# Kernel tuning notes

Measured on AMD Instinct MI355X. Metric: run time of the kernel, lower is better.

Reference implementation:

```python
import jax, jax.numpy as jnp
import numpy as np

B, P, D = 64, 196, 2048      # batch, num_pixels, encoder_dim
E, H, A = 512, 512, 512      # embed, hidden, attention dims
V, S = 32000, 22             # vocab, caption seq_len


def setup_inputs() -> dict:
    key = jax.random.key(0)
    ks = jax.random.split(key, 24)
    sc = 0.02
    features = jax.random.normal(ks[0], (B, P, D), jnp.float32)
    captions = jax.random.randint(ks[1], (S, B), 0, V)
    caption_lengths = jax.random.randint(ks[2], (B,), 3, S + 1)
    caption_lengths = caption_lengths.at[0].set(S)  # make max static = S
    p = lambda i, shp: sc * jax.random.normal(ks[i], shp, jnp.float32)
    return {
        "features": features,
        "captions": captions,
        "caption_lengths": caption_lengths,
        "emb_W": p(3, (V, E)),
        "We": p(4, (D, A)), "be": p(5, (A,)),
        "Wd": p(6, (H, A)), "bd": p(7, (A,)),
        "wf": p(8, (A, 1)), "bf": p(9, (1,)),
        "Wih": p(10, (4 * H, E + D)), "Whh": p(11, (4 * H, H)),
        "bih": p(12, (4 * H,)), "bhh": p(13, (4 * H,)),
        "Wh0": p(14, (D, H)), "bh0": p(15, (H,)),
        "Wc0": p(16, (D, H)), "bc0": p(17, (H,)),
        "Wbeta": p(18, (H, D)), "bbeta": p(19, (D,)),
        "Wout": p(20, (H, V)), "bout": p(21, (V,)),
    }


def reference(features, captions, caption_lengths, emb_W, We, be, Wd, bd, wf, bf,
              Wih, Whh, bih, bhh, Wh0, bh0, Wc0, bc0, Wbeta, bbeta, Wout, bout):
    # sort batch by caption length, descending
    sort_ind = jnp.argsort(-caption_lengths)
    lens = caption_lengths[sort_ind]
    enc = features[sort_ind]                     # [B,P,D]
    caps = captions.T[sort_ind]                  # [B,S]
    emb = emb_W[caps]                            # [B,S,E]
    mean_enc = enc.mean(axis=1)
    h0 = mean_enc @ Wh0 + bh0
    c0 = mean_enc @ Wc0 + bc0
    decode_lengths = lens - 1
    T = captions.shape[0] - 2                    # max(decode_lengths) - 1, static
    att1 = enc @ We + be                         # [B,P,A], step-invariant
    emb_t = jnp.moveaxis(emb[:, :T, :], 1, 0)    # [T,B,E]
    t_idx = jnp.arange(T)

    def step(carry, inp):
        h, c = carry
        e_t, t = inp
        att2 = h @ Wd + bd                                   # [B,A]
        scores = (jax.nn.relu(att1 + att2[:, None, :]) @ wf)[..., 0] + bf[0]  # [B,P]
        alpha = jax.nn.softmax(scores, axis=1)
        awe = jnp.einsum('bpd,bp->bd', enc, alpha)           # [B,D]
        gate = jax.nn.sigmoid(h @ Wbeta + bbeta)             # [B,D]
        x = jnp.concatenate([e_t, gate * awe], axis=1)       # [B,E+D]
        g = x @ Wih.T + bih + h @ Whh.T + bhh                # [B,4H]
        i, f, gg, o = jnp.split(g, 4, axis=1)                # torch LSTMCell gate order
        c_new = jax.nn.sigmoid(f) * c + jax.nn.sigmoid(i) * jnp.tanh(gg)
        h_new = jax.nn.sigmoid(o) * jnp.tanh(c_new)
        preds = h_new @ Wout + bout                          # [B,V] (dropout in eval = identity)
        m = (decode_lengths > t)[:, None].astype(preds.dtype)
        return (h_new, c_new), (preds * m, alpha * m)

    (_, _), (preds, alphas) = jax.lax.scan(step, (h0, c0), (emb_t, t_idx))
    predictions = jnp.moveaxis(preds, 0, 1)   # [B,T,V]
    alphas = jnp.moveaxis(alphas, 0, 1)       # [B,T,P]
    return predictions, caps, lens, alphas, sort_ind
```

## Files before the change

### kernel.cpp

```cpp
#include <hip/hip_runtime.h>
#include <stdint.h>

typedef short s16x8 __attribute__((ext_vector_type(8)));
typedef short s16x4 __attribute__((ext_vector_type(4)));
typedef float f32x4 __attribute__((ext_vector_type(4)));
typedef unsigned short u16;
typedef unsigned int u32;

#define DEV __device__ __forceinline__

DEV float bf2f(u16 v){ union{float f; unsigned u;} x; x.u = ((unsigned)v)<<16; return x.f; }
DEV u16 f2bf(float f){ union{float f; unsigned u;} x; x.f = f; unsigned r = x.u + 0x7fffu + ((x.u>>16)&1u); return (u16)(r>>16); }
DEV float sigm(float x){ return 1.f/(1.f + __expf(-x)); }

DEV u32  aL(const u32* p){ return __hip_atomic_load(p, __ATOMIC_RELAXED, __HIP_MEMORY_SCOPE_AGENT); }
DEV void aS(u32* p, u32 v){ __hip_atomic_store(p, v, __ATOMIC_RELAXED, __HIP_MEMORY_SCOPE_AGENT); }
DEV float aLf(const float* p){ return __hip_atomic_load(p, __ATOMIC_RELAXED, __HIP_MEMORY_SCOPE_AGENT); }
DEV void aSf(float* p, float v){ __hip_atomic_store(p, v, __ATOMIC_RELAXED, __HIP_MEMORY_SCOPE_AGENT); }


enum { EPI_F32=0, EPI_BF16=1, EPI_H0C0=2, EPI_PREDS=3 };

struct EpiParams {
  float* out0; long ldo;
  u16* outb;
  const float* bias0;
  const int* declen;
  float* c; u16* xh;
};

template<int BM, int BN, int EPI, bool SWAPXY, int SWZM>
__global__ __launch_bounds__(256) void gemm_bt(
    const u16* __restrict__ A, long lda,
    const u16* __restrict__ B, long ldb,
    int K, EpiParams ep)
{
  constexpr int MF = BM/64;
  constexpr int NF = BN/16;
  constexpr int CHA = BM*8, CH = CHA + BN*8;
  constexpr int NST = CH/256;
  __shared__ char smem[(BM+BN)*128];
  const int tid = threadIdx.x;
  const int w = tid>>6, lane = tid&63;

  long arow0, brow0;
  if constexpr (SWZM > 0) {
    int id = blockIdx.x, tot = gridDim.x;
    int q = tot>>3, r = tot&7, xcd = id&7, idx = id>>3;
    int cid = (xcd<r) ? xcd*(q+1)+idx : r*(q+1)+(xcd-r)*q+idx;
    arow0 = (long)(cid % SWZM)*BM; brow0 = (long)(cid / SWZM)*BN;
  } else if constexpr (SWAPXY) { arow0 = (long)blockIdx.x*BM; brow0 = (long)blockIdx.y*BN; }
  else { arow0 = (long)blockIdx.y*BM; brow0 = (long)blockIdx.x*BN; }

  const u16* gsrc[NST]; int ldst[NST];
  #pragma unroll
  for (int i=0;i<NST;++i){
    int c = i*256 + tid;
    if (i*256 < CHA){
      int row = c>>3, k16 = c&7;
      gsrc[i] = A + (arow0+row)*lda + k16*8;
      ldst[i] = row*128 + ((k16*16) ^ ((row&7)<<4));
    } else {
      int cb = c - CHA; int row = cb>>3, k16 = cb&7;
      gsrc[i] = B + (brow0+row)*ldb + k16*8;
      ldst[i] = BM*128 + row*128 + ((k16*16) ^ ((row&7)<<4));
    }
  }

  f32x4 acc[MF][NF];
  #pragma unroll
  for (int i=0;i<MF;++i)
    #pragma unroll
    for (int j=0;j<NF;++j) acc[i][j] = (f32x4){0.f,0.f,0.f,0.f};

  const int KT = K >> 6;
  s16x8 st[NST];
  #pragma unroll
  for (int i=0;i<NST;++i) st[i] = *(const s16x8*)(gsrc[i]);

  char* Al = smem;
  for (int kk=0; kk<KT; ++kk){
    #pragma unroll
    for (int i=0;i<NST;++i) *(s16x8*)(smem + ldst[i]) = st[i];
    __syncthreads();
    if (kk+1 < KT){
      long kb = (long)(kk+1)*64;
      #pragma unroll
      for (int i=0;i<NST;++i) st[i] = *(const s16x8*)(gsrc[i] + kb);
    }
    #pragma unroll
    for (int ks = 0; ks < 2; ++ks) {
      s16x8 af[MF], bfr[NF];
      const int kboff = ks*64 + ((lane>>4)<<4);
      #pragma unroll
      for (int mf=0; mf<MF; ++mf) {
        int r = w*(16*MF) + mf*16 + (lane&15);
        af[mf] = *(const s16x8*)(Al + r*128 + (kboff ^ ((r&7)<<4)));
      }
      #pragma unroll
      for (int nf=0; nf<NF; ++nf) {
        int r = nf*16 + (lane&15);
        bfr[nf] = *(const s16x8*)(Al + BM*128 + r*128 + (kboff ^ ((r&7)<<4)));
      }
      #pragma unroll
      for (int mf=0; mf<MF; ++mf)
        #pragma unroll
        for (int nf=0; nf<NF; ++nf)
          acc[mf][nf] = __builtin_amdgcn_mfma_f32_16x16x32_bf16(bfr[nf], af[mf], acc[mf][nf], 0,0,0);
    }
    __syncthreads();
  }

  #pragma unroll
  for (int mf=0; mf<MF; ++mf)
    #pragma unroll
    for (int nf=0; nf<NF; ++nf){
      long m = arow0 + w*(16*MF) + mf*16 + (lane&15);
      long n0 = brow0 + nf*16 + ((lane>>4)<<2);
      f32x4 bv = *(const f32x4*)&ep.bias0[n0];
      f32x4 v = acc[mf][nf] + bv;
      if constexpr (EPI == EPI_F32) {
        *(f32x4*)&ep.out0[m*ep.ldo + n0] = v;
      } else if constexpr (EPI == EPI_BF16) {
        u16 o[4];
        #pragma unroll
        for (int r=0;r<4;++r) o[r] = f2bf(v[r]);
        *(s16x4*)&ep.outb[m*ep.ldo + n0] = *(s16x4*)o;
      } else if constexpr (EPI == EPI_H0C0) {
        if (n0 < 512){
          u16 o[4];
          #pragma unroll
          for (int r=0;r<4;++r) o[r] = f2bf(v[r]);
          *(s16x4*)&ep.xh[m*2560 + 2048 + n0] = *(s16x4*)o;
        } else {
          *(f32x4*)&ep.c[m*512 + (n0-512)] = v;
        }
      } else {
        int tt = (int)(m>>6), b = (int)(m&63);
        if (ep.declen[b] > tt)
          *(f32x4*)&ep.out0[(long)b*640000 + (long)tt*32000 + n0] = v;
      }
    }
}

DEV void gsync(u32* flags, u32* epochw, u32 ep, int blk, int tid){
  __syncthreads();
  if (blk == 0){
    if (tid == 0) aS(flags, ep);
    if (tid < 256){
      while (aL(flags + tid*16) < ep) __builtin_amdgcn_s_sleep(4);
    }
    __syncthreads();
    if (tid == 0) aS(epochw, ep);
  } else {
    if (tid == 0){
      aS(flags + blk*16, ep);
      while (aL(epochw) < ep) __builtin_amdgcn_s_sleep(8);
    }
    __syncthreads();
  }
}

struct FusedArgs {
  const u16* att1; const u16* enc;
  const u16* wmisc; const u16* wcat2;
  const float* gst; const float* wf; const float* bfp;
  const int* declen; const float* bmisc; const int* nact;
  u16* xhA; u16* xhB; float* y0p;
  float* part; int* cnt; float* c; u16* hall;
  float* alph; u32* bar;
};

__global__ __launch_bounds__(512) void steps_fused(FusedArgs fa)
{
  __shared__ char smem[61440];
  __shared__ float wred[8];
  __shared__ int lastf;
  const int blk = blockIdx.x, tid = threadIdx.x;
  const int w = tid>>6, lane = tid&63;
  const int mstrip = w>>1, nhalf = w&1;
  u32* flags = fa.bar;
  u32* epochw = fa.bar + 4096;
  u32 ep = 0;

  for (int t=0; t<20; ++t){
    u16* cur = (t&1) ? fa.xhB : fa.xhA;
    u16* nxt = (t&1) ? fa.xhA : fa.xhB;
    u32* cur32 = (u32*)cur;
    u32* nxt32 = (u32*)nxt;

    if (blk < 80){
      const int brow0 = blk*32;
      f32x4 acc = {0,0,0,0};
      #pragma unroll
      for (int r=0; r<2; ++r){
        u32 sa[16];
        #pragma unroll
        for (int i=0;i<16;++i){
          int c = i*512 + tid;
          int row = c>>7, kp = c&127;
          sa[i] = aL(cur32 + (long)row*1280 + 1024 + r*128 + kp);
        }
        s16x8 sb[2];
        #pragma unroll
        for (int i=0;i<2;++i){
          int c = i*512 + tid;
          int row = c>>5, k16 = c&31;
          sb[i] = *(const s16x8*)(fa.wmisc + (long)(brow0+row)*512 + r*256 + k16*8);
        }
        #pragma unroll
        for (int i=0;i<16;++i){
          int c = i*512 + tid;
          int row = c>>7, kp = c&127;
          *(u32*)(smem + row*512 + ((kp*4) ^ ((row&7)<<4))) = sa[i];
        }
        #pragma unroll
        for (int i=0;i<2;++i){
          int c = i*512 + tid;
          int row = c>>5, k16 = c&31;
          *(s16x8*)(smem + 32768 + row*512 + ((k16*16) ^ ((row&7)<<4))) = sb[i];
        }
        __syncthreads();
        #pragma unroll
        for (int ks=0; ks<8; ++ks){
          int kboff = ks*64 + ((lane>>4)<<4);
          int ra = mstrip*16 + (lane&15);
          s16x8 af = *(const s16x8*)(smem + ra*512 + (kboff ^ ((ra&7)<<4)));
          int rb = nhalf*16 + (lane&15);
          s16x8 bf = *(const s16x8*)(smem + 32768 + rb*512 + (kboff ^ ((rb&7)<<4)));
          acc = __builtin_amdgcn_mfma_f32_16x16x32_bf16(bf, af, acc, 0,0,0);
        }
        __syncthreads();
      }
      int m = mstrip*16 + (lane&15);
      int n0 = brow0 + nhalf*16 + ((lane>>4)<<2);
      #pragma unroll
      for (int j=0;j<4;++j)
        aSf(fa.y0p + (long)m*2560 + n0 + j, acc[j] + fa.bmisc[n0+j]);
    }
    gsync(flags, epochw, ++ep, blk, tid);

    {
      const int b = blk>>2, s = blk&3;
      const int na = fa.nact[t];
      if (b >= na){
        if (s == 0){
          for (int i=tid; i<196; i+=512)
            fa.alph[((long)b*20 + t)*196 + i] = 0.f;
        }
      } else {
      float* att2p = (float*)smem;
      float* wfp   = att2p + 576;
      float* alps  = wfp + 576;
      float* awe_p = alps + 208;
      {
        int kg0 = tid>>6, j = tid&63;
        att2p[kg0*72 + j] = aLf(fa.y0p + (long)b*2560 + 2048 + tid);
        wfp[kg0*72 + j]   = fa.wf[tid];
      }
      __syncthreads();
      const float bfv = fa.bfp[0];
      const int pg = lane>>3, kg = lane&7;
      #pragma unroll
      for (int pass=0; pass<4; ++pass){
        int p = pass*64 + w*8 + pg;
        if (p < 196){
          const u16* ap = fa.att1 + (((long)(b*196 + p))<<9) + kg*64;
          float sa = 0.f;
          #pragma unroll
          for (int i=0;i<8;++i){
            s16x8 v = *(const s16x8*)(ap + i*8);
            #pragma unroll
            for (int q=0;q<8;++q){
              float x = bf2f((u16)v[q]) + att2p[kg*72 + i*8 + q];
              x = fmaxf(x, 0.f);
              sa += x * wfp[kg*72 + i*8 + q];
            }
          }
          sa += __shfl_xor(sa, 1);
          sa += __shfl_xor(sa, 2);
          sa += __shfl_xor(sa, 4);
          if (kg == 0) alps[p] = sa + bfv;
        }
      }
      __syncthreads();
      float v = (tid < 196) ? alps[tid] : -3.4e38f;
      float m8 = v;
      #pragma unroll
      for (int off=32; off; off>>=1) m8 = fmaxf(m8, __shfl_xor(m8, off));
      if (lane == 0) wred[w] = m8;
      __syncthreads();
      float mx = wred[0];
      #pragma unroll
      for (int i=1;i<8;++i) mx = fmaxf(mx, wred[i]);
      float e = (tid < 196) ? __expf(v - mx) : 0.f;
      float s8 = e;
      #pragma unroll
      for (int off=32; off; off>>=1) s8 += __shfl_xor(s8, off);
      __syncthreads();
      if (lane == 0) wred[w] = s8;
      __syncthreads();
      float den = wred[0]+wred[1]+wred[2]+wred[3]+wred[4]+wred[5]+wred[6]+wred[7];
      float inv = 1.f/den;
      if (tid < 196){
        float a = e*inv;
        alps[tid] = a;
        if (s==0) fa.alph[((long)b*20 + t)*196 + tid] = (fa.declen[b] > t) ? a : 0.f;
      }
      __syncthreads();
      const int d0 = s*512 + lane*8;
      const u16* ebase = fa.enc + (((long)b*196)<<11) + d0;
      float a8[8] = {0,0,0,0,0,0,0,0};
      int p = w;
      for (; p+24 < 196; p += 32){
        s16x8 e0 = *(const s16x8*)(ebase + ((long)p<<11));
        s16x8 e1 = *(const s16x8*)(ebase + ((long)(p+8)<<11));
        s16x8 e2 = *(const s16x8*)(ebase + ((long)(p+16)<<11));
        s16x8 e3 = *(const s16x8*)(ebase + ((long)(p+24)<<11));
        float a0 = alps[p], a1 = alps[p+8], a2 = alps[p+16], a3 = alps[p+24];
        #pragma unroll
        for (int q=0;q<8;++q) a8[q] += a0*bf2f((u16)e0[q]);
        #pragma unroll
        for (int q=0;q<8;++q) a8[q] += a1*bf2f((u16)e1[q]);
        #pragma unroll
        for (int q=0;q<8;++q) a8[q] += a2*bf2f((u16)e2[q]);
        #pragma unroll
        for (int q=0;q<8;++q) a8[q] += a3*bf2f((u16)e3[q]);
      }
      for (; p < 196; p += 8){
        s16x8 ev = *(const s16x8*)(ebase + ((long)p<<11));
        float a = alps[p];
        #pragma unroll
        for (int q=0;q<8;++q) a8[q] += a*bf2f((u16)ev[q]);
      }
      *(f32x4*)&awe_p[w*512 + lane*8]     = (f32x4){a8[0],a8[1],a8[2],a8[3]};
      *(f32x4*)&awe_p[w*512 + lane*8 + 4] = (f32x4){a8[4],a8[5],a8[6],a8[7]};
      __syncthreads();
      if (tid < 256){
        int c0 = 2*tid;
        float s0 = 0.f, s1 = 0.f;
        #pragma unroll
        for (int g=0; g<8; ++g){ s0 += awe_p[g*512 + c0]; s1 += awe_p[g*512 + c0 + 1]; }
        float g0 = sigm(aLf(fa.y0p + (long)b*2560 + s*512 + c0));
        float g1 = sigm(aLf(fa.y0p + (long)b*2560 + s*512 + c0 + 1));
        u32 pk = (u32)f2bf(g0*s0) | ((u32)f2bf(g1*s1) << 16);
        aS(cur32 + (long)b*1280 + s*256 + tid, pk);
      }
      __syncthreads();
      }
    }
    gsync(flags, epochw, ++ep, blk, tid);

    {
      const int ntile = blk>>2, split = blk&3;
      f32x4 acc = {0,0,0,0};
      #pragma unroll
      for (int r=0; r<2; ++r){
        const int kbw = split*640 + r*320;
        const int kbd = split*320 + r*160;
        u32 sa[20];
        #pragma unroll
        for (int i=0;i<20;++i){
          int c = i*512 + tid;
          int row = c/160, kp = c%160;
          sa[i] = aL(cur32 + (long)row*1280 + kbd + kp);
        }
        s16x8 sb[3];
        #pragma unroll
        for (int i=0;i<3;++i){
          int c = i*512 + tid;
          if (c < 1280){
            int row = c/40, k16 = c%40;
            sb[i] = *(const s16x8*)(fa.wcat2 + (long)(ntile*32+row)*2560 + kbw + k16*8);
          }
        }
        #pragma unroll
        for (int i=0;i<20;++i){
          int c = i*512 + tid;
          int row = c/160, kp = c%160;
          *(u32*)(smem + row*640 + ((kp*4) ^ ((row&7)<<4))) = sa[i];
        }
        #pragma unroll
        for (int i=0;i<3;++i){
          int c = i*512 + tid;
          if (c < 1280){
            int row = c/40, k16 = c%40;
            *(s16x8*)(smem + 40960 + row*640 + ((k16*16) ^ ((row&7)<<4))) = sb[i];
          }
        }
        __syncthreads();
        #pragma unroll
        for (int ks=0; ks<10; ++ks){
          int kboff = ks*64 + ((lane>>4)<<4);
          int ra = mstrip*16 + (lane&15);
          s16x8 af = *(const s16x8*)(smem + ra*640 + (kboff ^ ((ra&7)<<4)));
          int rb = nhalf*16 + (lane&15);
          s16x8 bf = *(const s16x8*)(smem + 40960 + rb*640 + (kboff ^ ((rb&7)<<4)));
          acc = __builtin_amdgcn_mfma_f32_16x16x32_bf16(bf, af, acc, 0,0,0);
        }
        __syncthreads();
      }
      {
        float* PS = fa.part + (long)split*(64*2048);
        int m = mstrip*16 + (lane&15);
        int n0 = ntile*32 + nhalf*16 + ((lane>>4)<<2);
        #pragma unroll
        for (int j=0;j<4;++j) aSf(PS + (long)m*2048 + n0 + j, acc[j]);
      }
      __syncthreads();
      if (tid==0){
        int v = __hip_atomic_fetch_add(fa.cnt + t*64 + ntile, 1,
                                       __ATOMIC_RELAXED, __HIP_MEMORY_SCOPE_AGENT);
        lastf = (v == 3);
      }
      __syncthreads();
      if (lastf && tid < 256){
        int b = tid>>2, jp = tid&3;
        u16 h2[2];
        #pragma unroll
        for (int jj=0; jj<2; ++jj){
          int jl = jp*2 + jj;
          int j = ntile*8 + jl;
          float g4[4];
          #pragma unroll
          for (int gi=0; gi<4; ++gi){
            long n = (long)ntile*32 + jl*4 + gi;
            float sg = fa.gst[((long)t*64 + b)*2048 + n];
            #pragma unroll
            for (int sp=0; sp<4; ++sp)
              sg += aLf(fa.part + (long)sp*(64*2048) + (long)b*2048 + n);
            g4[gi] = sg;
          }
          float cc = aLf(fa.c + b*512 + j);
          float cn = sigm(g4[1])*cc + sigm(g4[0])*tanhf(g4[2]);
          float hn = sigm(g4[3])*tanhf(cn);
          aSf(fa.c + b*512 + j, cn);
          h2[jj] = f2bf(hn);
        }
        u32 pk = (u32)h2[0] | ((u32)h2[1] << 16);
        aS(nxt32 + (long)b*1280 + 1024 + ntile*4 + jp, pk);
        *(u32*)&fa.hall[((long)t*64 + b)*512 + ntile*8 + jp*2] = pk;
      }
    }
    if (t < 19) gsync(flags, epochw, ++ep, blk, tid);
  }
}

__global__ __launch_bounds__(256) void transpose_bf16(
    const float* __restrict__ in, u16* __restrict__ out, int R, int C)
{
  __shared__ float t[64][65];
  const int bx = blockIdx.x*64, by = blockIdx.y*64;
  const int tx = threadIdx.x & 63, ty = threadIdx.x >> 6;
  #pragma unroll
  for (int i=0;i<16;++i){ int r = i*4+ty; t[r][tx] = in[(long)(by+r)*C + bx+tx]; }
  __syncthreads();
  #pragma unroll
  for (int i=0;i<16;++i){ int cc = i*4+ty; out[(long)(bx+cc)*R + by+tx] = f2bf(t[tx][cc]); }
}

__global__ void sort_k(const int* __restrict__ cl, const int* __restrict__ captions,
                       int* __restrict__ sidx, int* __restrict__ declen,
                       float* __restrict__ outCaps, float* __restrict__ outLens,
                       float* __restrict__ outSidx, int* __restrict__ cnt,
                       u32* __restrict__ bar, int* __restrict__ nact)
{
  __shared__ int s_idx[64];
  __shared__ int s_dl[64];
  int i = threadIdx.x;
  int li = cl[i];
  int rank = 0;
  for (int j=0;j<64;++j){ int lj = cl[j]; rank += (lj>li) || (lj==li && j<i); }
  s_idx[rank] = i;
  __syncthreads();
  int src = s_idx[i];
  sidx[i] = src;
  int L = cl[src];
  declen[i] = L - 1;
  s_dl[i] = L - 1;
  outLens[i] = (float)L;
  outSidx[i] = (float)src;
  for (int s=0;s<22;++s) outCaps[i*22+s] = (float)captions[s*64 + src];
  for (int s=0;s<20;++s) cnt[s*64 + i] = 0;
  for (int s=i; s<4160; s+=64) bar[s] = 0u;
  __syncthreads();
  if (i < 20){
    int c = 0;
    for (int j=0;j<64;++j) c += (s_dl[j] > i);
    nact[i] = c;
  }
}

__global__ __launch_bounds__(256) void prep_enc(
    const float* __restrict__ features, const int* __restrict__ sidx,
    u16* __restrict__ enc, u16* __restrict__ meanb)
{
  __shared__ float red[4][256];
  int b = blockIdx.x >> 3, oct = blockIdx.x & 7;
  int lv = threadIdx.x & 63, g = threadIdx.x >> 6;
  int d0 = oct*256 + lv*4;
  const float* src = features + (long)sidx[b]*(196*2048) + d0;
  float acc[4] = {0.f,0.f,0.f,0.f};
  for (int p=g; p<196; p+=4){
    f32x4 v = *(const f32x4*)(src + (long)p*2048);
    u16 o[4];
    #pragma unroll
    for (int q=0;q<4;++q){ acc[q] += v[q]; o[q] = f2bf(v[q]); }
    *(s16x4*)(enc + ((long)b*196 + p)*2048 + d0) = *(s16x4*)o;
  }
  #pragma unroll
  for (int q=0;q<4;++q) red[g][lv*4+q] = acc[q];
  __syncthreads();
  if (threadIdx.x < 64){
    u16 mo[4];
    #pragma unroll
    for (int q=0;q<4;++q){
      float s = red[0][threadIdx.x*4+q] + red[1][threadIdx.x*4+q]
              + red[2][threadIdx.x*4+q] + red[3][threadIdx.x*4+q];
      mo[q] = f2bf(s*(1.f/196.f));
    }
    *(s16x4*)(meanb + b*2048 + oct*256 + threadIdx.x*4) = *(s16x4*)mo;
  }
}

__global__ void emb_gather(const int* __restrict__ captions, const int* __restrict__ sidx,
                           const float* __restrict__ embW, u16* __restrict__ out)
{
  int idx = blockIdx.x*256 + threadIdx.x;
  int row = idx >> 6; int e0 = (idx & 63)*8;
  int t = row >> 6, b = row & 63;
  int tok = captions[t*64 + sidx[b]];
  const float* s = embW + (long)tok*512 + e0;
  f32x4 v0 = *(const f32x4*)s, v1 = *(const f32x4*)(s+4);
  u16 o[8];
  #pragma unroll
  for (int q=0;q<4;++q){ o[q] = f2bf(v0[q]); o[4+q] = f2bf(v1[q]); }
  *(s16x8*)(out + (long)row*512 + e0) = *(s16x8*)o;
}

__global__ void build_wcat2(const float* __restrict__ Wih, const float* __restrict__ Whh,
                            u16* __restrict__ out)
{
  long idx = (long)blockIdx.x*256 + threadIdx.x;
  int r = (int)(idx / 320);
  int kc = (int)(idx % 320) * 8;
  int j = r>>2, g = r&3;
  int orow = g*512 + j;
  const float* s = (kc < 2048) ? (Wih + (long)orow*2560 + 512 + kc)
                               : (Whh + (long)orow*512 + (kc - 2048));
  f32x4 v0 = *(const f32x4*)s, v1 = *(const f32x4*)(s+4);
  u16 o[8];
  #pragma unroll
  for (int q=0;q<4;++q){ o[q] = f2bf(v0[q]); o[4+q] = f2bf(v1[q]); }
  *(s16x8*)(out + (long)r*2560 + kc) = *(s16x8*)o;
}

__global__ void build_wihe(const float* __restrict__ Wih, u16* __restrict__ out)
{
  int idx = blockIdx.x*256 + threadIdx.x;
  int r = idx >> 6; int kc = (idx & 63)*8;
  int j = r>>2, g = r&3;
  const float* s = Wih + (long)(g*512+j)*2560 + kc;
  f32x4 v0 = *(const f32x4*)s, v1 = *(const f32x4*)(s+4);
  u16 o[8];
  #pragma unroll
  for (int q=0;q<4;++q){ o[q] = f2bf(v0[q]); o[4+q] = f2bf(v1[q]); }
  *(s16x8*)(out + (long)r*512 + kc) = *(s16x8*)o;
}

__global__ void build_bias(const float* bih, const float* bhh, const float* bbeta,
                           const float* bd, const float* bh0, const float* bc0,
                           float* bstat, float* bmisc, float* bhc)
{
  int idx = blockIdx.x*256 + threadIdx.x;
  if (idx < 2048){ int j = idx>>2, g = idx&3; bstat[idx] = bih[g*512+j] + bhh[g*512+j]; }
  else if (idx < 4608){ int k = idx-2048; bmisc[k] = (k<2048) ? bbeta[k] : bd[k-2048]; }
  else if (idx < 5632){ int k = idx-4608; bhc[k] = (k<512) ? bh0[k] : bc0[k-512]; }
}

static constexpr long OFF_ENC   = 0;
static constexpr long OFF_ATT1  = 51380224;
static constexpr long OFF_WOUTT = 64225280;
static constexpr long OFF_WET   = 96993280;
static constexpr long OFF_WMISC = 99090432;
static constexpr long OFF_WHC   = 101711872;
static constexpr long OFF_WCAT2 = 105906176;
static constexpr long OFF_WIHE  = 116391936;
static constexpr long OFF_EMBB  = 118489088;
static constexpr long OFF_GST   = 119799808;
static constexpr long OFF_HALL  = 130285568;
static constexpr long OFF_MEANB = 131596288;
static constexpr long OFF_XHA   = 131858432;
static constexpr long OFF_XHB   = 132186112;
static constexpr long OFF_C     = 132513792;
static constexpr long OFF_Y0P   = 132644864;
static constexpr long OFF_BSTAT = 133955584;
static constexpr long OFF_BMISC = 133963776;
static constexpr long OFF_BHC   = 133974016;
static constexpr long OFF_SIDX  = 133978112;
static constexpr long OFF_DECL  = 133978368;
static constexpr long OFF_CNT   = 133978624;
static constexpr long OFF_BAR   = 133983744;
static constexpr long OFF_NACT  = 134000384;
static constexpr long OFF_PART  = OFF_WHC;

extern "C" void kernel_launch(void* const* d_in, const int* in_sizes, int n_in,
                              void* d_out, int out_size, void* d_ws, size_t ws_size,
                              hipStream_t stream)
{
  (void)in_sizes; (void)n_in; (void)out_size; (void)ws_size;
  const float* features = (const float*)d_in[0];
  const int*   captions = (const int*)d_in[1];
  const int*   caplen   = (const int*)d_in[2];
  const float* embW     = (const float*)d_in[3];
  const float* We       = (const float*)d_in[4];
  const float* be       = (const float*)d_in[5];
  const float* Wd       = (const float*)d_in[6];
  const float* bd       = (const float*)d_in[7];
  const float* wf       = (const float*)d_in[8];
  const float* bfp      = (const float*)d_in[9];
  const float* Wih      = (const float*)d_in[10];
  const float* Whh      = (const float*)d_in[11];
  const float* bih      = (const float*)d_in[12];
  const float* bhh      = (const float*)d_in[13];
  const float* Wh0      = (const float*)d_in[14];
  const float* bh0      = (const float*)d_in[15];
  const float* Wc0      = (const float*)d_in[16];
  const float* bc0      = (const float*)d_in[17];
  const float* Wbeta    = (const float*)d_in[18];
  const float* bbeta    = (const float*)d_in[19];
  const float* Wout     = (const float*)d_in[20];
  const float* bout     = (const float*)d_in[21];

  char* ws = (char*)d_ws;
  u16*   enc   = (u16*)(ws + OFF_ENC);
  u16*   att1  = (u16*)(ws + OFF_ATT1);
  u16*   woutt = (u16*)(ws + OFF_WOUTT);
  u16*   wet   = (u16*)(ws + OFF_WET);
  u16*   wmisc = (u16*)(ws + OFF_WMISC);
  u16*   whc   = (u16*)(ws + OFF_WHC);
  u16*   wcat2 = (u16*)(ws + OFF_WCAT2);
  u16*   wihe  = (u16*)(ws + OFF_WIHE);
  u16*   embb  = (u16*)(ws + OFF_EMBB);
  float* gst   = (float*)(ws + OFF_GST);
  u16*   hall  = (u16*)(ws + OFF_HALL);
  u16*   meanb = (u16*)(ws + OFF_MEANB);
  u16*   xhA   = (u16*)(ws + OFF_XHA);
  u16*   xhB   = (u16*)(ws + OFF_XHB);
  float* cbuf  = (float*)(ws + OFF_C);
  float* y0p   = (float*)(ws + OFF_Y0P);
  float* bstat = (float*)(ws + OFF_BSTAT);
  float* bmisc = (float*)(ws + OFF_BMISC);
  float* bhc   = (float*)(ws + OFF_BHC);
  int*   sidx  = (int*)(ws + OFF_SIDX);
  int*   declen= (int*)(ws + OFF_DECL);
  int*   cnt   = (int*)(ws + OFF_CNT);
  u32*   bar   = (u32*)(ws + OFF_BAR);
  int*   nact  = (int*)(ws + OFF_NACT);
  float* part  = (float*)(ws + OFF_PART);

  float* outP    = (float*)d_out;
  float* outCaps = outP + 40960000;
  float* outLens = outCaps + 1408;
  float* outAlph = outLens + 64;
  float* outSidx = outAlph + 250880;

  sort_k<<<1,64,0,stream>>>(caplen, captions, sidx, declen, outCaps, outLens, outSidx, cnt, bar, nact);
  prep_enc<<<512,256,0,stream>>>(features, sidx, enc, meanb);
  emb_gather<<<320,256,0,stream>>>(captions, sidx, embW, embb);
  transpose_bf16<<<dim3(8,32),256,0,stream>>>(We,    wet,              2048, 512);
  transpose_bf16<<<dim3(32,8),256,0,stream>>>(Wbeta, wmisc,            512, 2048);
  transpose_bf16<<<dim3(8,8), 256,0,stream>>>(Wd,    wmisc + 2048*512, 512, 512);
  transpose_bf16<<<dim3(8,32),256,0,stream>>>(Wh0,   whc,              2048, 512);
  transpose_bf16<<<dim3(8,32),256,0,stream>>>(Wc0,   whc + 512*2048,   2048, 512);
  transpose_bf16<<<dim3(500,8),256,0,stream>>>(Wout, woutt,            512, 32000);
  build_wcat2<<<2560,256,0,stream>>>(Wih, Whh, wcat2);
  build_wihe<<<512,256,0,stream>>>(Wih, wihe);
  build_bias<<<22,256,0,stream>>>(bih,bhh,bbeta,bd,bh0,bc0,bstat,bmisc,bhc);

  { EpiParams ep{}; ep.bias0 = bhc; ep.xh = xhA; ep.c = cbuf;
    gemm_bt<64,64,EPI_H0C0,false,0><<<dim3(16,1),256,0,stream>>>(meanb, 2048, whc, 2048, 2048, ep); }
  { EpiParams ep{}; ep.outb = att1; ep.ldo = 512; ep.bias0 = be;
    gemm_bt<128,128,EPI_BF16,true,0><<<dim3(98,4),256,0,stream>>>(enc, 2048, wet, 2048, 2048, ep); }
  { EpiParams ep{}; ep.out0 = gst; ep.ldo = 2048; ep.bias0 = bstat;
    gemm_bt<128,64,EPI_F32,false,0><<<dim3(32,10),256,0,stream>>>(embb, 512, wihe, 512, 512, ep); }

  {
    FusedArgs fa;
    fa.att1 = att1; fa.enc = enc; fa.wmisc = wmisc; fa.wcat2 = wcat2;
    fa.gst = gst; fa.wf = wf; fa.bfp = bfp; fa.declen = declen; fa.bmisc = bmisc;
    fa.nact = nact;
    fa.xhA = xhA; fa.xhB = xhB; fa.y0p = y0p;
    fa.part = part; fa.cnt = cnt; fa.c = cbuf; fa.hall = hall;
    fa.alph = outAlph; fa.bar = bar;
    void* kargs[1] = { &fa };
    hipLaunchCooperativeKernel((const void*)steps_fused, dim3(256), dim3(512),
                               kargs, 0, stream);
  }

  { EpiParams ep{}; ep.out0 = outP; ep.bias0 = bout; ep.declen = declen;
    gemm_bt<128,128,EPI_PREDS,false,10><<<2500,256,0,stream>>>(hall, 512, woutt, 512, 512, ep); }
}
```

Measured before the change: 1.324 ms.

## Use per-step xh buffers, plain loads, nontemporal enc loads, remap block roles

Replaces the ping-pong xhA/xhB state buffers with twenty per-step buffers, so every step writes into fresh memory. This lets the GEMM phases read xh with plain (cacheable, vectorizable) loads instead of relaxed atomic loads without seeing stale cached data. The block-to-(batch,slice) mapping changes from interleaved to strided, which spreads each batch row's slices across different blocks and XCDs. Encoder loads in the attention-weighted sum become nontemporal to avoid polluting cache. Plain loads rely on caches not holding stale lines from earlier steps, and the extra workspace enlarges the memory footprint.

```diff
diff --git a/kernel.cpp b/kernel.cpp
--- a/kernel.cpp
+++ b/kernel.cpp
@@ -166,7 +166,7 @@
   const u16* wmisc; const u16* wcat2;
   const float* gst; const float* wf; const float* bfp;
   const int* declen; const float* bmisc; const int* nact;
-  u16* xhA; u16* xhB; float* y0p;
+  u16* xh20; float* y0p;
   float* part; int* cnt; float* c; u16* hall;
   float* alph; u32* bar;
 };
@@ -184,8 +184,8 @@
   u32 ep = 0;
 
   for (int t=0; t<20; ++t){
-    u16* cur = (t&1) ? fa.xhB : fa.xhA;
-    u16* nxt = (t&1) ? fa.xhA : fa.xhB;
+    u16* cur = fa.xh20 + (long)t*163840;
+    u16* nxt = cur + 163840;
     u32* cur32 = (u32*)cur;
     u32* nxt32 = (u32*)nxt;
 
@@ -199,7 +199,7 @@
         for (int i=0;i<16;++i){
           int c = i*512 + tid;
           int row = c>>7, kp = c&127;
-          sa[i] = aL(cur32 + (long)row*1280 + 1024 + r*128 + kp);
+          sa[i] = *(const u32*)(cur32 + (long)row*1280 + 1024 + r*128 + kp);
         }
         s16x8 sb[2];
         #pragma unroll
@@ -241,7 +241,7 @@
     gsync(flags, epochw, ++ep, blk, tid);
 
     {
-      const int b = blk>>2, s = blk&3;
+      const int b = blk & 63, s = blk >> 6;
       const int na = fa.nact[t];
       if (b >= na){
         if (s == 0){
@@ -313,10 +313,10 @@
       float a8[8] = {0,0,0,0,0,0,0,0};
       int p = w;
       for (; p+24 < 196; p += 32){
-        s16x8 e0 = *(const s16x8*)(ebase + ((long)p<<11));
-        s16x8 e1 = *(const s16x8*)(ebase + ((long)(p+8)<<11));
-        s16x8 e2 = *(const s16x8*)(ebase + ((long)(p+16)<<11));
-        s16x8 e3 = *(const s16x8*)(ebase + ((long)(p+24)<<11));
+        s16x8 e0 = __builtin_nontemporal_load((const s16x8*)(ebase + ((long)p<<11)));
+        s16x8 e1 = __builtin_nontemporal_load((const s16x8*)(ebase + ((long)(p+8)<<11)));
+        s16x8 e2 = __builtin_nontemporal_load((const s16x8*)(ebase + ((long)(p+16)<<11)));
+        s16x8 e3 = __builtin_nontemporal_load((const s16x8*)(ebase + ((long)(p+24)<<11)));
         float a0 = alps[p], a1 = alps[p+8], a2 = alps[p+16], a3 = alps[p+24];
         #pragma unroll
         for (int q=0;q<8;++q) a8[q] += a0*bf2f((u16)e0[q]);
@@ -328,7 +328,7 @@
         for (int q=0;q<8;++q) a8[q] += a3*bf2f((u16)e3[q]);
       }
       for (; p < 196; p += 8){
-        s16x8 ev = *(const s16x8*)(ebase + ((long)p<<11));
+        s16x8 ev = __builtin_nontemporal_load((const s16x8*)(ebase + ((long)p<<11)));
         float a = alps[p];
         #pragma unroll
         for (int q=0;q<8;++q) a8[q] += a*bf2f((u16)ev[q]);
@@ -352,7 +352,7 @@
     gsync(flags, epochw, ++ep, blk, tid);
 
     {
-      const int ntile = blk>>2, split = blk&3;
+      const int ntile = blk & 63, split = blk >> 6;
       f32x4 acc = {0,0,0,0};
       #pragma unroll
       for (int r=0; r<2; ++r){
@@ -363,7 +363,7 @@
         for (int i=0;i<20;++i){
           int c = i*512 + tid;
           int row = c/160, kp = c%160;
-          sa[i] = aL(cur32 + (long)row*1280 + kbd + kp);
+          sa[i] = *(const u32*)(cur32 + (long)row*1280 + kbd + kp);
         }
         s16x8 sb[3];
         #pragma unroll
@@ -590,8 +590,6 @@
 static constexpr long OFF_GST   = 119799808;
 static constexpr long OFF_HALL  = 130285568;
 static constexpr long OFF_MEANB = 131596288;
-static constexpr long OFF_XHA   = 131858432;
-static constexpr long OFF_XHB   = 132186112;
 static constexpr long OFF_C     = 132513792;
 static constexpr long OFF_Y0P   = 132644864;
 static constexpr long OFF_BSTAT = 133955584;
@@ -602,6 +600,7 @@
 static constexpr long OFF_CNT   = 133978624;
 static constexpr long OFF_BAR   = 133983744;
 static constexpr long OFF_NACT  = 134000384;
+static constexpr long OFF_XH20  = 134017024;
 static constexpr long OFF_PART  = OFF_WHC;
 
 extern "C" void kernel_launch(void* const* d_in, const int* in_sizes, int n_in,
@@ -645,8 +644,6 @@
   float* gst   = (float*)(ws + OFF_GST);
   u16*   hall  = (u16*)(ws + OFF_HALL);
   u16*   meanb = (u16*)(ws + OFF_MEANB);
-  u16*   xhA   = (u16*)(ws + OFF_XHA);
-  u16*   xhB   = (u16*)(ws + OFF_XHB);
   float* cbuf  = (float*)(ws + OFF_C);
   float* y0p   = (float*)(ws + OFF_Y0P);
   float* bstat = (float*)(ws + OFF_BSTAT);
@@ -657,6 +654,7 @@
   int*   cnt   = (int*)(ws + OFF_CNT);
   u32*   bar   = (u32*)(ws + OFF_BAR);
   int*   nact  = (int*)(ws + OFF_NACT);
+  u16*   xh20  = (u16*)(ws + OFF_XH20);
   float* part  = (float*)(ws + OFF_PART);
 
   float* outP    = (float*)d_out;
@@ -678,7 +676,7 @@
   build_wihe<<<512,256,0,stream>>>(Wih, wihe);
   build_bias<<<22,256,0,stream>>>(bih,bhh,bbeta,bd,bh0,bc0,bstat,bmisc,bhc);
 
-  { EpiParams ep{}; ep.bias0 = bhc; ep.xh = xhA; ep.c = cbuf;
+  { EpiParams ep{}; ep.bias0 = bhc; ep.xh = xh20; ep.c = cbuf;
     gemm_bt<64,64,EPI_H0C0,false,0><<<dim3(16,1),256,0,stream>>>(meanb, 2048, whc, 2048, 2048, ep); }
   { EpiParams ep{}; ep.outb = att1; ep.ldo = 512; ep.bias0 = be;
     gemm_bt<128,128,EPI_BF16,true,0><<<dim3(98,4),256,0,stream>>>(enc, 2048, wet, 2048, 2048, ep); }
@@ -690,7 +688,7 @@
     fa.att1 = att1; fa.enc = enc; fa.wmisc = wmisc; fa.wcat2 = wcat2;
     fa.gst = gst; fa.wf = wf; fa.bfp = bfp; fa.declen = declen; fa.bmisc = bmisc;
     fa.nact = nact;
-    fa.xhA = xhA; fa.xhB = xhB; fa.y0p = y0p;
+    fa.xh20 = xh20; fa.y0p = y0p;
     fa.part = part; fa.cnt = cnt; fa.c = cbuf; fa.hall = hall;
     fa.alph = outAlph; fa.bar = bar;
     void* kargs[1] = { &fa };
```

After: 1.320 ms. About the same (-0.3%).
